# Optimization experiments

Measured on AMD Instinct MI355X. Metric: run time of the kernel, lower is better.

The kernel has to match this reference:

```python
import jax, jax.numpy as jnp
import numpy as np

B, S, I, H, O, L = 64, 1024, 128, 512, 128, 2

def _gru_layer(x, h0, Wzx, Wzh, bz, Wrx, Wrh, br, Wgx, Wgh, bg):
    # Precompute input projections for all timesteps: (B,S,H)
    xz = jnp.einsum('bsi,ih->bsh', x, Wzx)
    xr = jnp.einsum('bsi,ih->bsh', x, Wrx)
    xg = jnp.einsum('bsi,ih->bsh', x, Wgx)
    def step(h, inp):
        xz_t, xr_t, xg_t = inp
        z = jax.nn.sigmoid(xz_t + h @ Wzh + bz)
        r = jax.nn.sigmoid(xr_t + h @ Wrh + br)
        g = jnp.tanh(xg_t + (r * h) @ Wgh + bg)
        h_new = z * h + (1.0 - z) * g
        return h_new, h_new
    # scan over time: move S to leading axis
    xs = (jnp.swapaxes(xz, 0, 1), jnp.swapaxes(xr, 0, 1), jnp.swapaxes(xg, 0, 1))
    hT, ys = jax.lax.scan(step, h0, xs)
    return jnp.swapaxes(ys, 0, 1), hT  # (B,S,H), (B,H)

def setup_inputs() -> dict:
    key = jax.random.key(0)
    ks = jax.random.split(key, 32)
    d = {}
    d['input'] = jax.random.normal(ks[0], (B, S, I), dtype=jnp.float32)
    d['hidden_state'] = jnp.zeros((B, L, H), dtype=jnp.float32)
    kidx = 1
    for layer in range(L):
        din = I if layer == 0 else H
        sx = 1.0 / np.sqrt(din)
        sh = 1.0 / np.sqrt(H)
        for gate in ('z', 'r', 'g'):
            d[f'W{gate}x{layer}'] = jax.random.uniform(ks[kidx], (din, H), jnp.float32, -sx, sx); kidx += 1
            d[f'W{gate}h{layer}'] = jax.random.uniform(ks[kidx], (H, H), jnp.float32, -sh, sh); kidx += 1
            d[f'b{gate}{layer}'] = jax.random.uniform(ks[kidx], (H,), jnp.float32, -sh, sh); kidx += 1
    so = 1.0 / np.sqrt(H)
    d['Wout'] = jax.random.uniform(ks[kidx], (H, O), jnp.float32, -so, so); kidx += 1
    d['bout'] = jax.random.uniform(ks[kidx], (O,), jnp.float32, -so, so)
    return d

def reference(input, hidden_state,
              Wzx0, Wzh0, bz0, Wrx0, Wrh0, br0, Wgx0, Wgh0, bg0,
              Wzx1, Wzh1, bz1, Wrx1, Wrh1, br1, Wgx1, Wgh1, bg1,
              Wout, bout):
    params = [
        (Wzx0, Wzh0, bz0, Wrx0, Wrh0, br0, Wgx0, Wgh0, bg0),
        (Wzx1, Wzh1, bz1, Wrx1, Wrh1, br1, Wgx1, Wgh1, bg1),
    ]
    x = input
    finals = []
    for layer in range(L):
        h0 = hidden_state[:, layer, :]
        x, hT = _gru_layer(x, h0, *params[layer])
        finals.append(hT)
    layer_output = jnp.einsum('bsh,ho->bso', x, Wout) + bout  # (B,S,O)
    hidden_out = jnp.stack(finals, axis=1)  # (B,L,H)
    return layer_output, hidden_out
```

## Files before the change

### kernel.cpp

```cpp
#include <hip/hip_runtime.h>
#include <cstdint>
#include <cstddef>

#define BDIM 256
#define NWG  256

constexpr int B_ = 64, S_ = 1024, I_ = 128, H_ = 512, O_ = 128;
constexpr size_t HB = (size_t)H_ * B_;

constexpr size_t Y1_OFF  = 0;
constexpr size_t Y2_OFF  = Y1_OFF + 2 * HB;
constexpr size_t RH0_OFF = Y2_OFF + 2 * HB;
constexpr size_t RH1_OFF = RH0_OFF + HB;
constexpr size_t Z0_OFF  = RH1_OFF + HB;
constexpr size_t Z1_OFF  = Z0_OFF + HB;
constexpr size_t BAR_OFF = Z1_OFF + HB;
constexpr size_t BAR_WORDS = 34 * 64;
constexpr size_t SLAB_TOT = BAR_OFF + BAR_WORDS;
constexpr size_t XT_OFF  = SLAB_TOT;
constexpr size_t XT_FLOATS = (size_t)S_ * I_ * B_;
constexpr size_t WS_NEED_XT_BYTES = (XT_OFF + XT_FLOATS) * 4;

__device__ __forceinline__ float4 llc_load4(const float* p) {
  const unsigned long long* q = (const unsigned long long*)p;
  unsigned long long lo = __hip_atomic_load(q,     __ATOMIC_RELAXED, __HIP_MEMORY_SCOPE_AGENT);
  unsigned long long hi = __hip_atomic_load(q + 1, __ATOMIC_RELAXED, __HIP_MEMORY_SCOPE_AGENT);
  union { unsigned long long u[2]; float4 v; } c;
  c.u[0] = lo; c.u[1] = hi;
  return c.v;
}
__device__ __forceinline__ float llc_loadf(const float* p) {
  unsigned int u = __hip_atomic_load((const unsigned int*)p, __ATOMIC_RELAXED,
                                     __HIP_MEMORY_SCOPE_AGENT);
  union { unsigned int u; float f; } c; c.u = u;
  return c.f;
}
__device__ __forceinline__ void llc_storef(float* p, float x) {
  union { float f; unsigned int u; } c; c.f = x;
  __hip_atomic_store((unsigned int*)p, c.u, __ATOMIC_RELAXED, __HIP_MEMORY_SCOPE_AGENT);
}

__global__ void k_init(const float* __restrict__ hidden, float* __restrict__ ws) {
  int idx = blockIdx.x * 256 + threadIdx.x;
  if (idx < (int)(2 * HB)) {
    int l = idx >> 15, r = idx & 32767;
    int k = r >> 6, b = r & 63;
    ws[(l ? Y2_OFF : Y1_OFF) + HB + r] = hidden[b * 1024 + l * 512 + k];
  } else if (idx < (int)(2 * HB + BAR_WORDS)) {
    ((unsigned int*)(ws + BAR_OFF))[idx - 2 * HB] = 0u;
  }
}

__global__ void k_transpose_x(const float* __restrict__ in, float* __restrict__ Xt) {
  const size_t NQ = (size_t)B_ * S_ * I_ / 4;
  for (size_t q = (size_t)blockIdx.x * blockDim.x + threadIdx.x; q < NQ;
       q += (size_t)gridDim.x * blockDim.x) {
    int i4 = (int)(q & 31);
    int t  = (int)((q >> 5) & 1023);
    int b  = (int)(q >> 15);
    float4 v = *(const float4*)(in + ((size_t)b * 1024 + t) * 128 + i4 * 4);
    float* dst = Xt + (size_t)t * 8192 + (size_t)(i4 * 4) * 64 + b;
    dst[0] = v.x; dst[64] = v.y; dst[128] = v.z; dst[192] = v.w;
  }
}

__device__ __forceinline__ void fmas(float4& a, float s, const float4 h) {
  a.x = fmaf(s, h.x, a.x); a.y = fmaf(s, h.y, a.y);
  a.z = fmaf(s, h.z, a.z); a.w = fmaf(s, h.w, a.w);
}

__device__ __forceinline__ void dotA8(const float* __restrict__ src, const float* __restrict__ wAp,
                                      int nch, int kt, int b4, float4* acc) {
  #pragma unroll 8
  for (int ch = 0; ch < nch; ++ch) {
    int kk = ch * 16 + kt;
    float4 h = llc_load4(src + (size_t)kk * 64 + b4);
    const float* wp = wAp + kk * 8;
    float4 w0 = *(const float4*)wp;
    float4 w1 = *(const float4*)(wp + 4);
    fmas(acc[0], w0.x, h); fmas(acc[1], w0.y, h); fmas(acc[2], w0.z, h); fmas(acc[3], w0.w, h);
    fmas(acc[4], w1.x, h); fmas(acc[5], w1.y, h); fmas(acc[6], w1.z, h); fmas(acc[7], w1.w, h);
  }
}

__device__ __forceinline__ void dotA8c(const float* __restrict__ src, const float* __restrict__ wAp,
                                       int nch, int kt, int b4, float4* acc) {
  #pragma unroll 8
  for (int ch = 0; ch < nch; ++ch) {
    int kk = ch * 16 + kt;
    float4 h = *(const float4*)(src + (size_t)kk * 64 + b4);
    const float* wp = wAp + kk * 8;
    float4 w0 = *(const float4*)wp;
    float4 w1 = *(const float4*)(wp + 4);
    fmas(acc[0], w0.x, h); fmas(acc[1], w0.y, h); fmas(acc[2], w0.z, h); fmas(acc[3], w0.w, h);
    fmas(acc[4], w1.x, h); fmas(acc[5], w1.y, h); fmas(acc[6], w1.z, h); fmas(acc[7], w1.w, h);
  }
}

__device__ __forceinline__ void dotA8x(const float* __restrict__ xin, int tau,
                                       const float* __restrict__ wAp, int kt, int b4, float4* acc) {
  #pragma unroll 2
  for (int ch = 0; ch < 8; ++ch) {
    int i = ch * 16 + kt;
    float4 h;
    h.x = xin[(size_t)(b4 + 0) * 131072 + tau * 128 + i];
    h.y = xin[(size_t)(b4 + 1) * 131072 + tau * 128 + i];
    h.z = xin[(size_t)(b4 + 2) * 131072 + tau * 128 + i];
    h.w = xin[(size_t)(b4 + 3) * 131072 + tau * 128 + i];
    const float* wp = wAp + i * 8;
    float4 w0 = *(const float4*)wp;
    float4 w1 = *(const float4*)(wp + 4);
    fmas(acc[0], w0.x, h); fmas(acc[1], w0.y, h); fmas(acc[2], w0.z, h); fmas(acc[3], w0.w, h);
    fmas(acc[4], w1.x, h); fmas(acc[5], w1.y, h); fmas(acc[6], w1.z, h); fmas(acc[7], w1.w, h);
  }
}

__device__ __forceinline__ void dotB4(const float* __restrict__ src, const float* __restrict__ wBp,
                                      int nch, int kt, int b4, float4* acc) {
  #pragma unroll 8
  for (int ch = 0; ch < nch; ++ch) {
    int kk = ch * 16 + kt;
    float4 h = llc_load4(src + (size_t)kk * 64 + b4);
    const float* wp = wBp + kk * 4;
    float4 w0 = *(const float4*)wp;
    fmas(acc[0], w0.x, h); fmas(acc[1], w0.y, h); fmas(acc[2], w0.z, h); fmas(acc[3], w0.w, h);
  }
}

__device__ __forceinline__ void dotB4c(const float* __restrict__ src, const float* __restrict__ wBp,
                                       int nch, int kt, int b4, float4* acc) {
  #pragma unroll 8
  for (int ch = 0; ch < nch; ++ch) {
    int kk = ch * 16 + kt;
    float4 h = *(const float4*)(src + (size_t)kk * 64 + b4);
    const float* wp = wBp + kk * 4;
    float4 w0 = *(const float4*)wp;
    fmas(acc[0], w0.x, h); fmas(acc[1], w0.y, h); fmas(acc[2], w0.z, h); fmas(acc[3], w0.w, h);
  }
}

__device__ __forceinline__ void dotB4x(const float* __restrict__ xin, int tau,
                                       const float* __restrict__ wBp, int kt, int b4, float4* acc) {
  #pragma unroll 2
  for (int ch = 0; ch < 8; ++ch) {
    int i = ch * 16 + kt;
    float4 h;
    h.x = xin[(size_t)(b4 + 0) * 131072 + tau * 128 + i];
    h.y = xin[(size_t)(b4 + 1) * 131072 + tau * 128 + i];
    h.z = xin[(size_t)(b4 + 2) * 131072 + tau * 128 + i];
    h.w = xin[(size_t)(b4 + 3) * 131072 + tau * 128 + i];
    const float* wp = wBp + i * 4;
    float4 w0 = *(const float4*)wp;
    fmas(acc[0], w0.x, h); fmas(acc[1], w0.y, h); fmas(acc[2], w0.z, h); fmas(acc[3], w0.w, h);
  }
}

__device__ __forceinline__ void grid_barrier(unsigned int* bar, unsigned int ph) {
  __syncthreads();
  asm volatile("" ::: "memory");
  if (threadIdx.x == 0) {
    const int g = (int)(blockIdx.x >> 4);
    unsigned int* grp_cnt  = bar + (size_t)g * 64;
    unsigned int* root_cnt = bar + 16 * 64;
    unsigned int* grp_gen  = bar + (size_t)(17 + g) * 64;
    unsigned int* root_gen = bar + 33 * 64;
    unsigned int r = __hip_atomic_fetch_add(grp_cnt, 1u, __ATOMIC_RELAXED, __HIP_MEMORY_SCOPE_AGENT);
    if (r == 16u * ph - 1u) {
      unsigned int rr = __hip_atomic_fetch_add(root_cnt, 1u, __ATOMIC_RELAXED, __HIP_MEMORY_SCOPE_AGENT);
      if (rr == 16u * ph - 1u) {
        __hip_atomic_store(root_gen, ph, __ATOMIC_RELAXED, __HIP_MEMORY_SCOPE_AGENT);
      } else {
        while (__hip_atomic_load(root_gen, __ATOMIC_RELAXED, __HIP_MEMORY_SCOPE_AGENT) < ph)
          __builtin_amdgcn_s_sleep(1);
      }
      __hip_atomic_store(grp_gen, ph, __ATOMIC_RELAXED, __HIP_MEMORY_SCOPE_AGENT);
    } else {
      while (__hip_atomic_load(grp_gen, __ATOMIC_RELAXED, __HIP_MEMORY_SCOPE_AGENT) < ph)
        __builtin_amdgcn_s_sleep(1);
    }
  }
  asm volatile("" ::: "memory");
  __syncthreads();
}

struct ScanArgs {
  float* ws;
  const float* xin;
  float* out;
  const float *Wzx0, *Wzh0, *bz0, *Wrx0, *Wrh0, *br0, *Wgx0, *Wgh0, *bg0;
  const float *Wzx1, *Wzh1, *bz1, *Wrx1, *Wrh1, *br1, *Wgx1, *Wgh1, *bg1;
  const float *Wout, *bout;
  int use_xt;
};

__launch_bounds__(BDIM, 1)
__global__ void k_scan(ScanArgs a) {
  float* ws = a.ws;
  unsigned int* bar = (unsigned int*)(ws + BAR_OFF);

  const int tid = threadIdx.x;
  const int wg  = blockIdx.x;
  const int kt  = tid >> 4;
  const int bq  = tid & 15;
  const int b4  = bq << 2;

  const int mA  = wg >> 6;
  const int lA  = mA >> 1;
  const int gA  = mA & 1;
  const int jA0 = (wg & 63) * 8;
  const int KA  = (mA < 2) ? 640 : 1024;
  const int mB  = wg >> 7;
  const int jB0 = (wg & 127) * 4;
  const int KB  = mB ? 1024 : 640;

  __shared__ float wA[8192];
  __shared__ float wB[4096];
  __shared__ float wO[512];
  __shared__ float pA[9 * 64 * 17];

  {
    const float* A0 = lA ? (gA ? a.Wrx1 : a.Wzx1) : (gA ? a.Wrh0 : a.Wzh0);
    const float* A1 = lA ? (gA ? a.Wrh1 : a.Wzh1) : (gA ? a.Wrx0 : a.Wzx0);
    for (int idx = tid; idx < KA * 8; idx += BDIM) {
      int k = idx >> 3, c = idx & 7;
      wA[idx] = (k < 512) ? A0[k * 512 + jA0 + c] : A1[(k - 512) * 512 + jA0 + c];
    }
    const float* B0 = mB ? a.Wgx1 : a.Wgh0;
    const float* B1 = mB ? a.Wgh1 : a.Wgx0;
    for (int idx = tid; idx < KB * 4; idx += BDIM) {
      int k = idx >> 2, c = idx & 3;
      wB[idx] = (k < 512) ? B0[k * 512 + jB0 + c] : B1[(k - 512) * 512 + jB0 + c];
    }
    if (wg < 128)
      for (int idx = tid; idx < 512; idx += BDIM) wO[idx] = a.Wout[(size_t)idx * 128 + wg];
  }
  const float* bAv = lA ? (gA ? a.br1 : a.bz1) : (gA ? a.br0 : a.bz0);
  const float biasA_0 = bAv[jA0 + (tid >> 6)];
  const float biasA_1 = bAv[jA0 + 4 + (tid >> 6)];
  const float biasB_0 = (mB ? a.bg1 : a.bg0)[jB0 + (tid >> 6)];
  const float boutW = (wg < 128) ? a.bout[wg] : 0.f;
  __syncthreads();

  const float* XT = ws + XT_OFF;
  unsigned int ph = 1;

  for (int tau = 0; tau <= S_ + 1; ++tau) {
    const bool doL0 = (tau < S_);
    const bool doL1 = (tau >= 1) && (tau <= S_);
    const int slotP = (tau + 1) & 1;
    const int slotQ = tau & 1;
    const float* y1p = ws + Y1_OFF + (size_t)slotP * HB;
    const float* y2p = ws + Y2_OFF + (size_t)slotQ * HB;
    float* y1w = ws + Y1_OFF + (size_t)slotQ * HB;
    float* y2w = ws + Y2_OFF + (size_t)slotP * HB;

    const bool actA = lA ? doL1 : doL0;
    float4 acc[8];
    #pragma unroll
    for (int c = 0; c < 8; ++c) acc[c] = make_float4(0.f, 0.f, 0.f, 0.f);
    if (actA) {
      dotA8(y1p, wA, 32, kt, b4, acc);
      if (mA < 2) {
        if (a.use_xt) dotA8c(XT + (size_t)tau * 8192, wA + 512 * 8, 8, kt, b4, acc);
        else          dotA8x(a.xin, tau, wA + 512 * 8, kt, b4, acc);
      } else {
        dotA8(y2p, wA + 512 * 8, 32, kt, b4, acc);
      }
    }
    const bool doOut = (tau >= 2) && (wg < 128);
    float4 accO = make_float4(0.f, 0.f, 0.f, 0.f);
    if (doOut) {
      #pragma unroll 8
      for (int ch = 0; ch < 32; ++ch) {
        int kk = ch * 16 + kt;
        float4 h = llc_load4(y2p + (size_t)kk * 64 + b4);
        fmas(accO, wO[kk], h);
      }
    }
    if (actA) {
      #pragma unroll
      for (int c = 0; c < 8; ++c) {
        float pv[4] = {acc[c].x, acc[c].y, acc[c].z, acc[c].w};
        #pragma unroll
        for (int j = 0; j < 4; ++j) pA[(c * 64 + b4 + j) * 17 + kt] = pv[j];
      }
    }
    if (doOut) {
      float pv[4] = {accO.x, accO.y, accO.z, accO.w};
      #pragma unroll
      for (int j = 0; j < 4; ++j) pA[(512 + b4 + j) * 17 + kt] = pv[j];
    }
    __syncthreads();
    if (actA) {
      #pragma unroll
      for (int r = 0; r < 2; ++r) {
        int idx = tid + (r << 8);
        int c = idx >> 6, b = idx & 63;
        float s = r ? biasA_1 : biasA_0;
        #pragma unroll
        for (int q = 0; q < 16; ++q) s += pA[(c * 64 + b) * 17 + q];
        float v = 1.0f / (1.0f + __expf(-s));
        size_t jb = (size_t)(jA0 + c) * 64 + b;
        if (gA == 0) {
          llc_storef(ws + (lA ? Z1_OFF : Z0_OFF) + jb, v);
        } else {
          const float* hpsl = lA ? y2p : y1p;
          float hp = llc_loadf(hpsl + jb);
          llc_storef(ws + (lA ? RH1_OFF : RH0_OFF) + jb, v * hp);
        }
      }
    }
    if (doOut && tid < 64) {
      float s = boutW;
      #pragma unroll
      for (int q = 0; q < 16; ++q) s += pA[(512 + tid) * 17 + q];
      a.out[((size_t)tid * 1024 + (tau - 2)) * 128 + wg] = s;
    }

    grid_barrier(bar, ph++);

    const bool actB = mB ? doL1 : doL0;
    float4 accB[4];
    #pragma unroll
    for (int c = 0; c < 4; ++c) accB[c] = make_float4(0.f, 0.f, 0.f, 0.f);
    if (actB) {
      const float* r0 = mB ? y1p : (ws + RH0_OFF);
      dotB4(r0, wB, 32, kt, b4, accB);
      if (mB) {
        dotB4(ws + RH1_OFF, wB + 512 * 4, 32, kt, b4, accB);
      } else {
        if (a.use_xt) dotB4c(XT + (size_t)tau * 8192, wB + 512 * 4, 8, kt, b4, accB);
        else          dotB4x(a.xin, tau, wB + 512 * 4, kt, b4, accB);
      }
      #pragma unroll
      for (int c = 0; c < 4; ++c) {
        float pv[4] = {accB[c].x, accB[c].y, accB[c].z, accB[c].w};
        #pragma unroll
        for (int j = 0; j < 4; ++j) pA[(c * 64 + b4 + j) * 17 + kt] = pv[j];
      }
    }
    __syncthreads();
    if (actB) {
      int c = tid >> 6, b = tid & 63;
      float s = biasB_0;
      #pragma unroll
      for (int q = 0; q < 16; ++q) s += pA[(c * 64 + b) * 17 + q];
      float g = tanhf(s);
      size_t jb = (size_t)(jB0 + c) * 64 + b;
      float z  = llc_loadf(ws + (mB ? Z1_OFF : Z0_OFF) + jb);
      float hp = llc_loadf((mB ? y2p : y1p) + jb);
      float hn = fmaf(z, hp - g, g);
      llc_storef((mB ? y2w : y1w) + jb, hn);
    }

    grid_barrier(bar, ph++);
  }
}

__global__ void k_hidden(const float* __restrict__ ws, float* __restrict__ out) {
  int idx = blockIdx.x * 256 + threadIdx.x;
  int b = idx >> 10, rem = idx & 1023, l = rem >> 9, j = rem & 511;
  const float* src = ws + (l ? Y2_OFF : Y1_OFF) + HB + (size_t)j * 64 + b;
  out[(size_t)B_ * S_ * O_ + idx] = *src;
}

extern "C" void kernel_launch(void* const* d_in, const int* in_sizes, int n_in,
                              void* d_out, int out_size, void* d_ws, size_t ws_size,
                              hipStream_t stream) {
  const float* input  = (const float*)d_in[0];
  const float* hidden = (const float*)d_in[1];
  const float* Wzx0 = (const float*)d_in[2],  *Wzh0 = (const float*)d_in[3],  *bz0 = (const float*)d_in[4];
  const float* Wrx0 = (const float*)d_in[5],  *Wrh0 = (const float*)d_in[6],  *br0 = (const float*)d_in[7];
  const float* Wgx0 = (const float*)d_in[8],  *Wgh0 = (const float*)d_in[9],  *bg0 = (const float*)d_in[10];
  const float* Wzx1 = (const float*)d_in[11], *Wzh1 = (const float*)d_in[12], *bz1 = (const float*)d_in[13];
  const float* Wrx1 = (const float*)d_in[14], *Wrh1 = (const float*)d_in[15], *br1 = (const float*)d_in[16];
  const float* Wgx1 = (const float*)d_in[17], *Wgh1 = (const float*)d_in[18], *bg1 = (const float*)d_in[19];
  const float* Wout = (const float*)d_in[20], *bout = (const float*)d_in[21];
  float* ws = (float*)d_ws;
  float* out = (float*)d_out;

  const int use_xt = (ws_size >= WS_NEED_XT_BYTES) ? 1 : 0;

  k_init<<<265, BDIM, 0, stream>>>(hidden, ws);
  if (use_xt) k_transpose_x<<<2048, BDIM, 0, stream>>>(input, ws + XT_OFF);

  ScanArgs sa{ws, input, out,
              Wzx0, Wzh0, bz0, Wrx0, Wrh0, br0, Wgx0, Wgh0, bg0,
              Wzx1, Wzh1, bz1, Wrx1, Wrh1, br1, Wgx1, Wgh1, bg1,
              Wout, bout, use_xt};
  k_scan<<<dim3(NWG), dim3(BDIM), 0, stream>>>(sa);

  k_hidden<<<256, 256, 0, stream>>>(ws, out);
}
```

Baseline: 16.75 ms.

## Hoist r-independent candidate-gate dot products before the grid barrier and fuse output projection

The candidate-gate terms that do not depend on r*h move into the pre-barrier phase. For layer 0 that is the x·Wgx part, and for layer 1 it is the y1·Wgx1 part. They are fused into the same loops that already load those activations for the z/r gates, so the post-barrier phase only does the r*h dot product. The output projection moves from layer-0 workgroups to layer-1 workgroups and is fused with their y2 loads, removing a separate pass over y2. This shortens the serial work after each grid barrier and rebalances the pre-barrier load. In exchange it costs extra registers for the live accumulators and puts more FMAs on the layer-1 workgroups.

```diff
diff --git a/kernel.cpp b/kernel.cpp
--- a/kernel.cpp
+++ b/kernel.cpp
@@ -70,9 +70,9 @@
 }
 
 __device__ __forceinline__ void dotA8(const float* __restrict__ src, const float* __restrict__ wAp,
-                                      int nch, int kt, int b4, float4* acc) {
+                                      int kt, int b4, float4* acc) {
   #pragma unroll 8
-  for (int ch = 0; ch < nch; ++ch) {
+  for (int ch = 0; ch < 32; ++ch) {
     int kk = ch * 16 + kt;
     float4 h = llc_load4(src + (size_t)kk * 64 + b4);
     const float* wp = wAp + kk * 8;
@@ -83,22 +83,65 @@
   }
 }
 
-__device__ __forceinline__ void dotA8c(const float* __restrict__ src, const float* __restrict__ wAp,
-                                       int nch, int kt, int b4, float4* acc) {
+__device__ __forceinline__ void fusedL1r1(const float* __restrict__ src,
+                                          const float* __restrict__ wAp,
+                                          const float* __restrict__ wBp,
+                                          int kt, int b4, float4* acc, float4* accB) {
   #pragma unroll 8
-  for (int ch = 0; ch < nch; ++ch) {
+  for (int ch = 0; ch < 32; ++ch) {
     int kk = ch * 16 + kt;
-    float4 h = *(const float4*)(src + (size_t)kk * 64 + b4);
+    float4 h = llc_load4(src + (size_t)kk * 64 + b4);
     const float* wp = wAp + kk * 8;
     float4 w0 = *(const float4*)wp;
     float4 w1 = *(const float4*)(wp + 4);
     fmas(acc[0], w0.x, h); fmas(acc[1], w0.y, h); fmas(acc[2], w0.z, h); fmas(acc[3], w0.w, h);
     fmas(acc[4], w1.x, h); fmas(acc[5], w1.y, h); fmas(acc[6], w1.z, h); fmas(acc[7], w1.w, h);
-  }
-}
-
-__device__ __forceinline__ void dotA8x(const float* __restrict__ xin, int tau,
-                                       const float* __restrict__ wAp, int kt, int b4, float4* acc) {
+    const float* gp = wBp + kk * 4;
+    float4 g0 = *(const float4*)gp;
+    fmas(accB[0], g0.x, h); fmas(accB[1], g0.y, h); fmas(accB[2], g0.z, h); fmas(accB[3], g0.w, h);
+  }
+}
+
+__device__ __forceinline__ void fusedL1r2(const float* __restrict__ src,
+                                          const float* __restrict__ wAp2,
+                                          const float* __restrict__ wOp,
+                                          int kt, int b4, float4* acc, float4& accO) {
+  #pragma unroll 8
+  for (int ch = 0; ch < 32; ++ch) {
+    int kk = ch * 16 + kt;
+    float4 h = llc_load4(src + (size_t)kk * 64 + b4);
+    const float* wp = wAp2 + kk * 8;
+    float4 w0 = *(const float4*)wp;
+    float4 w1 = *(const float4*)(wp + 4);
+    fmas(acc[0], w0.x, h); fmas(acc[1], w0.y, h); fmas(acc[2], w0.z, h); fmas(acc[3], w0.w, h);
+    fmas(acc[4], w1.x, h); fmas(acc[5], w1.y, h); fmas(acc[6], w1.z, h); fmas(acc[7], w1.w, h);
+    fmas(accO, wOp[kk], h);
+  }
+}
+
+__device__ __forceinline__ void fusedL0x(const float* __restrict__ src,
+                                         const float* __restrict__ wAp2,
+                                         const float* __restrict__ wBp2,
+                                         int kt, int b4, float4* acc, float4* accB) {
+  #pragma unroll 8
+  for (int ch = 0; ch < 8; ++ch) {
+    int i = ch * 16 + kt;
+    float4 h = *(const float4*)(src + (size_t)i * 64 + b4);
+    const float* wp = wAp2 + i * 8;
+    float4 w0 = *(const float4*)wp;
+    float4 w1 = *(const float4*)(wp + 4);
+    fmas(acc[0], w0.x, h); fmas(acc[1], w0.y, h); fmas(acc[2], w0.z, h); fmas(acc[3], w0.w, h);
+    fmas(acc[4], w1.x, h); fmas(acc[5], w1.y, h); fmas(acc[6], w1.z, h); fmas(acc[7], w1.w, h);
+    const float* gp = wBp2 + i * 4;
+    float4 g0 = *(const float4*)gp;
+    fmas(accB[0], g0.x, h); fmas(accB[1], g0.y, h); fmas(accB[2], g0.z, h); fmas(accB[3], g0.w, h);
+  }
+}
+
+__device__ __forceinline__ void fusedL0xf(const float* __restrict__ xin, int tau,
+                                          const float* __restrict__ wAp2,
+                                          const float* __restrict__ wBp2,
+                                          int kt, int b4, float4* acc, float4* accB) {
   #pragma unroll 2
   for (int ch = 0; ch < 8; ++ch) {
     int i = ch * 16 + kt;
@@ -107,49 +150,24 @@
     h.y = xin[(size_t)(b4 + 1) * 131072 + tau * 128 + i];
     h.z = xin[(size_t)(b4 + 2) * 131072 + tau * 128 + i];
     h.w = xin[(size_t)(b4 + 3) * 131072 + tau * 128 + i];
-    const float* wp = wAp + i * 8;
+    const float* wp = wAp2 + i * 8;
     float4 w0 = *(const float4*)wp;
     float4 w1 = *(const float4*)(wp + 4);
     fmas(acc[0], w0.x, h); fmas(acc[1], w0.y, h); fmas(acc[2], w0.z, h); fmas(acc[3], w0.w, h);
     fmas(acc[4], w1.x, h); fmas(acc[5], w1.y, h); fmas(acc[6], w1.z, h); fmas(acc[7], w1.w, h);
+    const float* gp = wBp2 + i * 4;
+    float4 g0 = *(const float4*)gp;
+    fmas(accB[0], g0.x, h); fmas(accB[1], g0.y, h); fmas(accB[2], g0.z, h); fmas(accB[3], g0.w, h);
   }
 }
 
 __device__ __forceinline__ void dotB4(const float* __restrict__ src, const float* __restrict__ wBp,
-                                      int nch, int kt, int b4, float4* acc) {
+                                      int kt, int b4, float4* acc) {
   #pragma unroll 8
-  for (int ch = 0; ch < nch; ++ch) {
+  for (int ch = 0; ch < 32; ++ch) {
     int kk = ch * 16 + kt;
     float4 h = llc_load4(src + (size_t)kk * 64 + b4);
     const float* wp = wBp + kk * 4;
-    float4 w0 = *(const float4*)wp;
-    fmas(acc[0], w0.x, h); fmas(acc[1], w0.y, h); fmas(acc[2], w0.z, h); fmas(acc[3], w0.w, h);
-  }
-}
-
-__device__ __forceinline__ void dotB4c(const float* __restrict__ src, const float* __restrict__ wBp,
-                                       int nch, int kt, int b4, float4* acc) {
-  #pragma unroll 8
-  for (int ch = 0; ch < nch; ++ch) {
-    int kk = ch * 16 + kt;
-    float4 h = *(const float4*)(src + (size_t)kk * 64 + b4);
-    const float* wp = wBp + kk * 4;
-    float4 w0 = *(const float4*)wp;
-    fmas(acc[0], w0.x, h); fmas(acc[1], w0.y, h); fmas(acc[2], w0.z, h); fmas(acc[3], w0.w, h);
-  }
-}
-
-__device__ __forceinline__ void dotB4x(const float* __restrict__ xin, int tau,
-                                       const float* __restrict__ wBp, int kt, int b4, float4* acc) {
-  #pragma unroll 2
-  for (int ch = 0; ch < 8; ++ch) {
-    int i = ch * 16 + kt;
-    float4 h;
-    h.x = xin[(size_t)(b4 + 0) * 131072 + tau * 128 + i];
-    h.y = xin[(size_t)(b4 + 1) * 131072 + tau * 128 + i];
-    h.z = xin[(size_t)(b4 + 2) * 131072 + tau * 128 + i];
-    h.w = xin[(size_t)(b4 + 3) * 131072 + tau * 128 + i];
-    const float* wp = wBp + i * 4;
     float4 w0 = *(const float4*)wp;
     fmas(acc[0], w0.x, h); fmas(acc[1], w0.y, h); fmas(acc[2], w0.z, h); fmas(acc[3], w0.w, h);
   }
@@ -212,6 +230,7 @@
   const int mB  = wg >> 7;
   const int jB0 = (wg & 127) * 4;
   const int KB  = mB ? 1024 : 640;
+  const int oc  = wg - 128;
 
   __shared__ float wA[8192];
   __shared__ float wB[4096];
@@ -231,14 +250,14 @@
       int k = idx >> 2, c = idx & 3;
       wB[idx] = (k < 512) ? B0[k * 512 + jB0 + c] : B1[(k - 512) * 512 + jB0 + c];
     }
-    if (wg < 128)
-      for (int idx = tid; idx < 512; idx += BDIM) wO[idx] = a.Wout[(size_t)idx * 128 + wg];
+    if (wg >= 128)
+      for (int idx = tid; idx < 512; idx += BDIM) wO[idx] = a.Wout[(size_t)idx * 128 + oc];
   }
   const float* bAv = lA ? (gA ? a.br1 : a.bz1) : (gA ? a.br0 : a.bz0);
   const float biasA_0 = bAv[jA0 + (tid >> 6)];
   const float biasA_1 = bAv[jA0 + 4 + (tid >> 6)];
   const float biasB_0 = (mB ? a.bg1 : a.bg0)[jB0 + (tid >> 6)];
-  const float boutW = (wg < 128) ? a.bout[wg] : 0.f;
+  const float boutW = (wg >= 128) ? a.bout[oc] : 0.f;
   __syncthreads();
 
   const float* XT = ws + XT_OFF;
@@ -255,21 +274,25 @@
     float* y2w = ws + Y2_OFF + (size_t)slotP * HB;
 
     const bool actA = lA ? doL1 : doL0;
+    const bool doOut = (tau >= 2) && (wg >= 128);
     float4 acc[8];
+    float4 accB[4];
+    float4 accO = make_float4(0.f, 0.f, 0.f, 0.f);
     #pragma unroll
     for (int c = 0; c < 8; ++c) acc[c] = make_float4(0.f, 0.f, 0.f, 0.f);
+    #pragma unroll
+    for (int c = 0; c < 4; ++c) accB[c] = make_float4(0.f, 0.f, 0.f, 0.f);
+
     if (actA) {
-      dotA8(y1p, wA, 32, kt, b4, acc);
       if (mA < 2) {
-        if (a.use_xt) dotA8c(XT + (size_t)tau * 8192, wA + 512 * 8, 8, kt, b4, acc);
-        else          dotA8x(a.xin, tau, wA + 512 * 8, kt, b4, acc);
+        dotA8(y1p, wA, kt, b4, acc);
+        if (a.use_xt) fusedL0x(XT + (size_t)tau * 8192, wA + 512 * 8, wB + 512 * 4, kt, b4, acc, accB);
+        else          fusedL0xf(a.xin, tau, wA + 512 * 8, wB + 512 * 4, kt, b4, acc, accB);
       } else {
-        dotA8(y2p, wA + 512 * 8, 32, kt, b4, acc);
-      }
-    }
-    const bool doOut = (tau >= 2) && (wg < 128);
-    float4 accO = make_float4(0.f, 0.f, 0.f, 0.f);
-    if (doOut) {
+        fusedL1r1(y1p, wA, wB, kt, b4, acc, accB);
+        fusedL1r2(y2p, wA + 512 * 8, wO, kt, b4, acc, accO);
+      }
+    } else if (tau == S_ + 1 && wg >= 128) {
       #pragma unroll 8
       for (int ch = 0; ch < 32; ++ch) {
         int kk = ch * 16 + kt;
@@ -277,6 +300,7 @@
         fmas(accO, wO[kk], h);
       }
     }
+
     if (actA) {
       #pragma unroll
       for (int c = 0; c < 8; ++c) {
@@ -314,24 +338,15 @@
       float s = boutW;
       #pragma unroll
       for (int q = 0; q < 16; ++q) s += pA[(512 + tid) * 17 + q];
-      a.out[((size_t)tid * 1024 + (tau - 2)) * 128 + wg] = s;
+      a.out[((size_t)tid * 1024 + (tau - 2)) * 128 + oc] = s;
     }
 
     grid_barrier(bar, ph++);
 
     const bool actB = mB ? doL1 : doL0;
-    float4 accB[4];
-    #pragma unroll
-    for (int c = 0; c < 4; ++c) accB[c] = make_float4(0.f, 0.f, 0.f, 0.f);
     if (actB) {
-      const float* r0 = mB ? y1p : (ws + RH0_OFF);
-      dotB4(r0, wB, 32, kt, b4, accB);
-      if (mB) {
-        dotB4(ws + RH1_OFF, wB + 512 * 4, 32, kt, b4, accB);
-      } else {
-        if (a.use_xt) dotB4c(XT + (size_t)tau * 8192, wB + 512 * 4, 8, kt, b4, accB);
-        else          dotB4x(a.xin, tau, wB + 512 * 4, kt, b4, accB);
-      }
+      if (mB == 0) dotB4(ws + RH0_OFF, wB, kt, b4, accB);
+      else         dotB4(ws + RH1_OFF, wB + 512 * 4, kt, b4, accB);
       #pragma unroll
       for (int c = 0; c < 4; ++c) {
         float pv[4] = {accB[c].x, accB[c].y, accB[c].z, accB[c].w};
```

New measurement: 18.28 ms. 1.09x slower.
